# Kernel optimization log

Measured on AMD Instinct MI355X. Metric: run time of the kernel, lower is better.

Reference implementation:

```python
import jax, jax.numpy as jnp
import numpy as np

NHEADS = 16

def setup_inputs() -> dict:
    key = jax.random.key(0)
    ks = jax.random.split(key, 5)
    C = 1024
    d = C // NHEADS
    x  = jax.random.normal(ks[0], (2, 2048, C), dtype=jnp.float32)
    sc = 1.0 / np.sqrt(C)
    wq = jax.random.normal(ks[1], (C, C), dtype=jnp.float32) * sc
    wk = jax.random.normal(ks[2], (C, C), dtype=jnp.float32) * sc
    wv = jax.random.normal(ks[3], (C, C), dtype=jnp.float32) * sc
    wo = jax.random.normal(ks[4], (d, C), dtype=jnp.float32) * (1.0 / np.sqrt(d))
    return {"x": x, "wq": wq, "wk": wk, "wv": wv, "wo": wo}

def reference(x, wq, wk, wv, wo):
    B, T, C = x.shape
    H = NHEADS
    d = C // H

    def split_heads(y):
        return y.reshape(B, T, H, d).transpose(0, 2, 1, 3)  # [B,H,T,d]

    Q = split_heads(x @ wq)
    K = split_heads(x @ wk)
    V = split_heads(x @ wv)

    # scores[b,h,q,k]
    prod = jnp.einsum('bhqd,bhkd->bhqk', Q, K) / np.sqrt(d)

    # ALiBi bias: offset[h, q, k] = (k - q) * 2**(-8*(h+1)/H)
    idx = jnp.arange(T)
    slopes = jnp.exp2(-8.0 * (jnp.arange(H, dtype=jnp.float32) + 1.0) / H)
    bias = (idx[None, :] - idx[:, None]).astype(x.dtype) * slopes[:, None, None]
    prod = prod + bias[None]

    # causal tril mask: keep k <= q
    keep = idx[None, :] <= idx[:, None]  # [T_q, T_k]
    prod = jnp.where(keep[None, None], prod, -jnp.inf)

    # NOTE: original uses F.softmax(prod, 2) -> softmax over the QUERY axis.
    attention_weights = jax.nn.softmax(prod, axis=2)
    attention_output = jnp.einsum('bhqk,bhkd->bhqd', attention_weights, V)

    # per-head wo projection then sum over heads == (sum over heads) @ wo (linear)
    outputs = attention_output.sum(axis=1) @ wo  # [B,T,C]
    return x + outputs
```

## Files before the change

kernel.cpp:

```cpp
#include <hip/hip_runtime.h>
#include <math.h>

#define NB 2
#define NH 16
#define NT 2048
#define ND 64
#define NC 1024
#define L2E 1.44269504f

typedef __attribute__((ext_vector_type(4))) float f32x4;
typedef __attribute__((ext_vector_type(8))) short short8;
typedef __attribute__((ext_vector_type(4))) short short4_t;
typedef __attribute__((ext_vector_type(8))) unsigned short ushort8;
typedef __attribute__((ext_vector_type(4))) unsigned short ushort4_t;

#define GLOAD_LDS(gp, lp)                                                \
    __builtin_amdgcn_global_load_lds(                                    \
        (const __attribute__((address_space(1))) void*)(gp),             \
        (__attribute__((address_space(3))) void*)(lp), 16, 0, 0)

__device__ __forceinline__ int sigma_p(int p) {
    return 4 * ((p >> 3) & 3) + (p & 3) + 16 * ((p >> 2) & 1) + 32 * (p >> 5);
}

__device__ __forceinline__ unsigned short f2bf(float f) {
    unsigned u = __builtin_bit_cast(unsigned, f);
    unsigned r = (u + 0x7FFFu + ((u >> 16) & 1u)) >> 16;
    return (unsigned short)r;
}

__device__ __forceinline__ unsigned cvtpk_bf16(float lo, float hi) {
    unsigned r;
    asm("v_cvt_pk_bf16_f32 %0, %1, %2" : "=v"(r) : "v"(lo), "v"(hi));
    return r;
}

__device__ __forceinline__ f32x4 mfma16(short8 a, short8 b, f32x4 c) {
    return __builtin_amdgcn_mfma_f32_16x16x32_bf16(a, b, c, 0, 0, 0);
}

__device__ __forceinline__ short8 frag_load(const unsigned short* rowp, int g, int half) {
    short8 v;
    short4_t lo = *(const short4_t*)(rowp + 4 * g + 32 * half);
    short4_t hi = *(const short4_t*)(rowp + 4 * g + 16 + 32 * half);
    #pragma unroll
    for (int j = 0; j < 4; ++j) { v[j] = lo[j]; v[4 + j] = hi[j]; }
    return v;
}

__device__ __forceinline__ short8 frag_g(const unsigned short* rowp, int g, int half) {
    return *(const short8*)(rowp + 8 * g + 32 * half);
}

__device__ __forceinline__ short8 frag_swz128(const unsigned short* tile, int row, int g, int half) {
    const char* p = (const char*)tile + row * 128 + (((g + 4 * half) ^ (row & 7)) << 4);
    return *(const short8*)p;
}

__global__ __launch_bounds__(256) void cvt_x(const float* __restrict__ src,
                                             unsigned short* __restrict__ dst, int n4) {
    int i = blockIdx.x * 256 + threadIdx.x;
    if (i >= n4) return;
    const int blk = i >> 4, c4 = i & 15;
    const int gg = (c4 >> 1) & 3, bb = c4 & 1, hh = c4 >> 3;
    f32x4 v = ((const f32x4*)src)[blk * 16 + gg + 4 * bb + 8 * hh];
    ushort4_t o;
    #pragma unroll
    for (int j = 0; j < 4; ++j) o[j] = f2bf(v[j]);
    ((ushort4_t*)dst)[i] = o;
}

__global__ __launch_bounds__(256) void cvtT3(const float* __restrict__ w0,
                                             const float* __restrict__ w1,
                                             const float* __restrict__ w2,
                                             unsigned short* __restrict__ Wt_all) {
    __shared__ __align__(16) float T[64][68];
    const float* W = (blockIdx.z == 0) ? w0 : ((blockIdx.z == 1) ? w1 : w2);
    unsigned short* Wt = Wt_all + (size_t)blockIdx.z * NC * NC;
    const int tid = threadIdx.x;
    const int k0 = blockIdx.x * 64, n0 = blockIdx.y * 64;
    #pragma unroll
    for (int p = 0; p < 4; ++p) {
        int r = 16 * p + (tid >> 4);
        int c = (tid & 15) * 4;
        *(f32x4*)&T[r][c] = *(const f32x4*)&W[(size_t)(k0 + r) * NC + n0 + c];
    }
    __syncthreads();
    const int nr = tid >> 2, kc = (tid & 3) * 16;
    ushort8 o0, o1;
    #pragma unroll
    for (int j = 0; j < 8; ++j) o0[j] = f2bf(T[sigma_p(kc + j)][nr]);
    #pragma unroll
    for (int j = 0; j < 8; ++j) o1[j] = f2bf(T[sigma_p(kc + 8 + j)][nr]);
    unsigned short* q = Wt + (size_t)(n0 + nr) * NC + k0 + kc;
    *(ushort8*)q       = o0;
    *(ushort8*)(q + 8) = o1;
}

__global__ __launch_bounds__(256) void cvtT_wo(const float* __restrict__ W,
                                               unsigned short* __restrict__ Wt) {
    __shared__ __align__(16) float T[64][68];
    const int tid = threadIdx.x;
    const int n0 = blockIdx.y * 64;
    #pragma unroll
    for (int p = 0; p < 4; ++p) {
        int r = 16 * p + (tid >> 4);
        int c = (tid & 15) * 4;
        *(f32x4*)&T[r][c] = *(const f32x4*)&W[(size_t)r * NC + n0 + c];
    }
    __syncthreads();
    const int nr = tid >> 2, kc = (tid & 3) * 16;
    ushort8 o0, o1;
    #pragma unroll
    for (int j = 0; j < 8; ++j) { o0[j] = f2bf(T[kc + j][nr]); o1[j] = f2bf(T[kc + 8 + j][nr]); }
    unsigned short* q = Wt + (size_t)(n0 + nr) * ND + kc;
    *(ushort8*)q       = o0;
    *(ushort8*)(q + 8) = o1;
}

__global__ __launch_bounds__(256) void gemm_qkv(const unsigned short* __restrict__ Xh,
                                                const unsigned short* __restrict__ Wt_all,
                                                unsigned short* __restrict__ dst_all) {
    __shared__ __align__(16) unsigned short Xs[2][8192];
    __shared__ __align__(16) unsigned short Ws[2][8192];
    const int tid = threadIdx.x;
    const int lane = tid & 63, w = tid >> 6;
    const int g = lane >> 4, l15 = lane & 15;
    const int wr = w >> 1, wc = w & 1;
    const int subrow = lane >> 3;
    const int src_off = (((lane & 7) ^ subrow) << 4);
    const int m0 = blockIdx.x * 128;
    const int which = blockIdx.y >> 3;
    const int n0 = (blockIdx.y & 7) * 128;
    const unsigned short* Wt = Wt_all + (size_t)which * NC * NC;
    unsigned short* dst = dst_all + (size_t)which * (NB * NH * NT * ND);

    f32x4 acc[4][4] = {};

    auto stage = [&](int buf, int kk) {
        #pragma unroll
        for (int i = 0; i < 4; ++i) {
            const int r0 = 8 * w + 32 * i;
            const char* xs = (const char*)Xh + (((size_t)(m0 + r0 + subrow) * NC + kk) << 1) + src_off;
            GLOAD_LDS(xs, (char*)&Xs[buf][r0 * 64]);
            const char* ws = (const char*)Wt + (((size_t)(n0 + r0 + subrow) * NC + kk) << 1) + src_off;
            GLOAD_LDS(ws, (char*)&Ws[buf][r0 * 64]);
        }
    };

    stage(0, 0);
    asm volatile("s_waitcnt vmcnt(0)" ::: "memory");
    __builtin_amdgcn_s_barrier();
    int cur = 0;

    for (int kk = 0; kk < NC; kk += 64) {
        if (kk + 64 < NC) stage(cur ^ 1, kk + 64);
        short8 a[4][2], b[4][2];
        #pragma unroll
        for (int mr = 0; mr < 4; ++mr) {
            a[mr][0] = frag_swz128(Xs[cur], 64 * wr + 16 * mr + l15, g, 0);
            a[mr][1] = frag_swz128(Xs[cur], 64 * wr + 16 * mr + l15, g, 1);
        }
        #pragma unroll
        for (int nc = 0; nc < 4; ++nc) {
            b[nc][0] = frag_swz128(Ws[cur], 64 * wc + 16 * nc + l15, g, 0);
            b[nc][1] = frag_swz128(Ws[cur], 64 * wc + 16 * nc + l15, g, 1);
        }
        #pragma unroll
        for (int mr = 0; mr < 4; ++mr)
            #pragma unroll
            for (int nc = 0; nc < 4; ++nc) {
                acc[mr][nc] = mfma16(a[mr][0], b[nc][0], acc[mr][nc]);
                acc[mr][nc] = mfma16(a[mr][1], b[nc][1], acc[mr][nc]);
            }
        asm volatile("s_waitcnt vmcnt(0)" ::: "memory");
        __builtin_amdgcn_s_barrier();
        cur ^= 1;
    }

    #pragma unroll
    for (int mr = 0; mr < 4; ++mr) {
        #pragma unroll
        for (int nc = 0; nc < 4; ++nc) {
            const int n = n0 + 64 * wc + 16 * nc + l15;
            const int hh = n >> 6;
            const int dd = (which < 2)
                ? 32 * (nc >> 1) + 8 * (l15 >> 2) + 4 * (nc & 1) + (l15 & 3)
                : 16 * nc + l15;
            #pragma unroll
            for (int r = 0; r < 4; ++r) {
                const int m = m0 + 64 * wr + 16 * mr + 4 * g + r;
                const int bb = m >> 11, tt = m & (NT - 1);
                dst[(((size_t)bb * NH + hh) * NT + tt) * ND + dd] = f2bf(acc[mr][nc][r]);
            }
        }
    }
}

__global__ __launch_bounds__(256) void transpose_v(const unsigned short* __restrict__ Vh,
                                                   unsigned short* __restrict__ Vt) {
    __shared__ __align__(16) unsigned short T[64][72];
    const int tid = threadIdx.x;
    const int bh = blockIdx.y;
    const int t0 = blockIdx.x * 64;
    const int srow = tid >> 2, scol = (tid & 3) * 16;
    const unsigned short* p = Vh + ((size_t)bh * NT + t0 + srow) * ND + scol;
    *(ushort8*)&T[srow][scol]     = *(const ushort8*)p;
    *(ushort8*)&T[srow][scol + 8] = *(const ushort8*)(p + 8);
    __syncthreads();
    ushort8 o0, o1;
    #pragma unroll
    for (int j = 0; j < 8; ++j) o0[j] = T[sigma_p(scol + j)][srow];
    #pragma unroll
    for (int j = 0; j < 8; ++j) o1[j] = T[sigma_p(scol + 8 + j)][srow];
    unsigned short* q = Vt + ((size_t)bh * ND + srow) * NT + t0 + scol;
    *(ushort8*)q       = o0;
    *(ushort8*)(q + 8) = o1;
}

__global__ __launch_bounds__(256) void colstats(const unsigned short* __restrict__ Qh,
                                                const unsigned short* __restrict__ Kh,
                                                float* __restrict__ Lout) {
    __shared__ __align__(16) unsigned short Qs[3][4096];
    const int tid = threadIdx.x;
    const int lane = tid & 63, w = tid >> 6;
    const int g = lane >> 4, l15 = lane & 15;
    const int subrow = lane >> 3;
    const int src_off = (((lane & 7) ^ subrow) << 4);
    const int lin = blockIdx.x + 16 * blockIdx.y;
    const int xcd = lin & 7, idx = lin >> 3;
    const int bh = xcd * 4 + (idx & 3);
    const int j = idx >> 2;
    const int jA = j, jB = 31 - j;
    const int hh = bh & (NH - 1);
    const float slL2 = exp2f(-0.5f * (float)(hh + 1)) * L2E;
    const float C1 = 0.125f * L2E;
    const float s16 = 16.f * slL2;

    const int K0A = 64 * jA, K0B = 64 * jB;
    const unsigned short* krA = Kh + ((size_t)bh * NT + K0A + 16 * w + l15) * ND;
    const unsigned short* krB = Kh + ((size_t)bh * NT + K0B + 16 * w + l15) * ND;
    const short8 akA0 = frag_g(krA, g, 0), akA1 = frag_g(krA, g, 1);
    const short8 akB0 = frag_g(krB, g, 0), akB1 = frag_g(krB, g, 1);
    const int kA0 = K0A + 16 * w + 4 * g;
    const int kB0 = K0B + 16 * w + 4 * g;

    const char* Qbase = (const char*)(Qh + (size_t)bh * NT * ND);
    auto stage = [&](int buf, int q0) {
        const char* qs = Qbase + (size_t)(q0 + 16 * w + subrow) * 128 + src_off;
        char* qd = (char*)&Qs[buf][16 * w * 64];
        GLOAD_LDS(qs, qd);
        GLOAD_LDS(qs + 1024, qd + 1024);
    };

    f32x4 accA = {}, accB = {};
    float rs[4];
    #pragma unroll
    for (int r = 0; r < 4; ++r) rs[r] = (float)r * slL2;

    stage(0, 64 * jA);
    stage(1, 64 * (jA + 1));
    int cur = 0, nxt = 2;

    auto strip = [&](const short8* qf, const short8& a0, const short8& a1,
                     f32x4& acc, float b0, bool mask) {
        #pragma unroll
        for (int q4 = 0; q4 < 4; ++q4) {
            f32x4 d = {};
            __builtin_amdgcn_s_setprio(1);
            d = mfma16(a0, qf[2 * q4], d);
            d = mfma16(a1, qf[2 * q4 + 1], d);
            __builtin_amdgcn_s_setprio(0);
            #pragma unroll
            for (int r = 0; r < 4; ++r) {
                float e = exp2f(fmaf(d[r], C1, b0 + rs[r]));
                if (mask && (16 * q4 + l15 < 16 * w + 4 * g + r)) e = 0.f;
                acc[r] += e;
            }
            b0 -= s16;
        }
    };

    for (int qt = jA; qt < 32; ++qt) {
        if (qt < 31) asm volatile("s_waitcnt vmcnt(2)" ::: "memory");
        else         asm volatile("s_waitcnt vmcnt(0)" ::: "memory");
        __builtin_amdgcn_s_barrier();
        if (qt + 2 < 32) stage(nxt, 64 * (qt + 2));
        const unsigned short* tile = Qs[cur];
        short8 qf[8];
        #pragma unroll
        for (int q4 = 0; q4 < 4; ++q4) {
            qf[2 * q4]     = frag_swz128(tile, 16 * q4 + l15, g, 0);
            qf[2 * q4 + 1] = frag_swz128(tile, 16 * q4 + l15, g, 1);
        }
        const int q0 = 64 * qt;
        strip(qf, akA0, akA1, accA, (float)(kA0 - q0 - l15) * slL2, qt == jA);
        if (qt >= jB)
            strip(qf, akB0, akB1, accB, (float)(kB0 - q0 - l15) * slL2, qt == jB);
        cur = (cur == 2) ? 0 : cur + 1;
        nxt = (nxt == 2) ? 0 : nxt + 1;
    }
    #pragma unroll
    for (int off = 1; off <= 8; off <<= 1) {
        #pragma unroll
        for (int r = 0; r < 4; ++r) {
            accA[r] += __shfl_xor(accA[r], off);
            accB[r] += __shfl_xor(accB[r], off);
        }
    }
    if (l15 == 0) {
        #pragma unroll
        for (int r = 0; r < 4; ++r) {
            Lout[(size_t)bh * NT + kA0 + r] = log2f(accA[r]);
            Lout[(size_t)bh * NT + kB0 + r] = log2f(accB[r]);
        }
    }
}

__global__ __launch_bounds__(256) void attn_pv(const unsigned short* __restrict__ Qh,
                                               const unsigned short* __restrict__ Kh,
                                               const unsigned short* __restrict__ Vt,
                                               const float* __restrict__ Lc,
                                               float* __restrict__ att) {
    __shared__ __align__(16) unsigned short Ks[3][4096];
    __shared__ __align__(16) unsigned short Vs[3][4096];
    __shared__ __align__(16) float Ls[NT];
    const int tid = threadIdx.x;
    const int lane = tid & 63, w = tid >> 6;
    const int g = lane >> 4, l15 = lane & 15;
    const int subrow = lane >> 3;
    const int src_off = (((lane & 7) ^ subrow) << 4);
    const int lin = blockIdx.x + 16 * blockIdx.y;
    const int xcd = lin & 7, idx = lin >> 3;
    const int bh = xcd * 4 + (idx & 3);
    const int j = idx >> 2;
    const int jA = j, jB = 31 - j;
    const int Q0A = 64 * jA, Q0B = 64 * jB;
    const int qA = Q0A + 16 * w + l15;
    const int qB = Q0B + 16 * w + l15;
    const int hh = bh & (NH - 1);
    const int bb = bh >> 4;
    const float slL2 = exp2f(-0.5f * (float)(hh + 1)) * L2E;
    const float C1 = 0.125f * L2E;

    short8 bqA0, bqA1, bqB0, bqB1;
    {
        const unsigned short* qr = Qh + ((size_t)bh * NT + qA) * ND;
        bqA0 = frag_g(qr, g, 0);
        bqA1 = frag_g(qr, g, 1);
        qr = Qh + ((size_t)bh * NT + qB) * ND;
        bqB0 = frag_g(qr, g, 0);
        bqB1 = frag_g(qr, g, 1);
    }

    auto stageKV = [&](int buf, int K0) {
        const char* ksrc = (const char*)Kh + (size_t)((size_t)bh * NT + K0 + 16 * w + subrow) * 128 + src_off;
        char* kdst = (char*)&Ks[buf][16 * w * 64];
        GLOAD_LDS(ksrc, kdst);
        GLOAD_LDS(ksrc + 1024, kdst + 1024);
        const char* vsrc = (const char*)Vt + ((((size_t)bh * ND + 16 * w + subrow) * NT + K0) << 1) + src_off;
        char* vdst = (char*)&Vs[buf][16 * w * 64];
        GLOAD_LDS(vsrc, vdst);
        GLOAD_LDS(vsrc + 8 * NT * 2, vdst + 1024);
    };

    stageKV(0, 0);
    stageKV(1, 64);
    {
        const f32x4* Lsrc = (const f32x4*)(Lc + (size_t)bh * NT);
        const int nv = (jB + 1) * 16;
        for (int i = tid; i < nv; i += 256) {
            f32x4 v = Lsrc[i];
            float kb = (float)(4 * i);
            #pragma unroll
            for (int c = 0; c < 4; ++c) v[c] -= (kb + (float)c) * slL2;
            ((f32x4*)Ls)[i] = v;
        }
    }
    asm volatile("s_waitcnt lgkmcnt(0)" ::: "memory");
    int cur = 0, nxt = 2;

    f32x4 oA[4] = {}, oB[4] = {};
    const float qsA = (float)qA * slL2;
    const float qsB = (float)qB * slL2;

    auto dostrip = [&](const short8* kf, const short8* vf,
                       const short8& q0f, const short8& q1f, f32x4 (&o)[4],
                       float qsc, int q, int K0, bool mask) {
        f32x4 pacc[4];
        __builtin_amdgcn_s_setprio(1);
        #pragma unroll
        for (int s4 = 0; s4 < 4; ++s4) {
            f32x4 d = {};
            d = mfma16(kf[2 * s4], q0f, d);
            d = mfma16(kf[2 * s4 + 1], q1f, d);
            pacc[s4] = d;
        }
        __builtin_amdgcn_s_setprio(0);
        union { unsigned u[4]; short8 s; } pa[2];
        #pragma unroll
        for (int s4 = 0; s4 < 4; ++s4) {
            f32x4 Lf = *(const f32x4*)&Ls[K0 + 16 * s4 + 4 * g];
            float p[4];
            #pragma unroll
            for (int r = 0; r < 4; ++r)
                p[r] = exp2f(fmaf(pacc[s4][r], C1, -(Lf[r] + qsc)));
            if (mask) {
                #pragma unroll
                for (int r = 0; r < 4; ++r)
                    if (K0 + 16 * s4 + 4 * g + r > q) p[r] = 0.f;
            }
            pa[s4 >> 1].u[2 * (s4 & 1)]     = cvtpk_bf16(p[0], p[1]);
            pa[s4 >> 1].u[2 * (s4 & 1) + 1] = cvtpk_bf16(p[2], p[3]);
        }
        __builtin_amdgcn_s_setprio(1);
        #pragma unroll
        for (int n = 0; n < 4; ++n) {
            o[n] = mfma16(pa[0].s, vf[2 * n], o[n]);
            o[n] = mfma16(pa[1].s, vf[2 * n + 1], o[n]);
        }
        __builtin_amdgcn_s_setprio(0);
    };

    for (int kt = 0; kt <= jB; ++kt) {
        if (kt < jB) asm volatile("s_waitcnt vmcnt(4)" ::: "memory");
        else         asm volatile("s_waitcnt vmcnt(0)" ::: "memory");
        __builtin_amdgcn_s_barrier();
        if (kt + 2 <= jB) stageKV(nxt, 64 * (kt + 2));
        const int K0 = 64 * kt;
        short8 kf[8], vf[8];
        #pragma unroll
        for (int s4 = 0; s4 < 4; ++s4) {
            kf[2 * s4]     = frag_swz128(Ks[cur], 16 * s4 + l15, g, 0);
            kf[2 * s4 + 1] = frag_swz128(Ks[cur], 16 * s4 + l15, g, 1);
            vf[2 * s4]     = frag_swz128(Vs[cur], 16 * s4 + l15, g, 0);
            vf[2 * s4 + 1] = frag_swz128(Vs[cur], 16 * s4 + l15, g, 1);
        }
        dostrip(kf, vf, bqB0, bqB1, oB, qsB, qB, K0, kt == jB);
        if (kt <= jA)
            dostrip(kf, vf, bqA0, bqA1, oA, qsA, qA, K0, kt == jA);
        cur = (cur == 2) ? 0 : cur + 1;
        nxt = (nxt == 2) ? 0 : nxt + 1;
    }
    #pragma unroll
    for (int n = 0; n < 4; ++n) {
        #pragma unroll
        for (int r = 0; r < 4; ++r) {
            att[(((size_t)bb * NT + Q0A + 16 * w + 4 * g + r) * NH + hh) * ND + 16 * n + l15] = oA[n][r];
            att[(((size_t)bb * NT + Q0B + 16 * w + 4 * g + r) * NH + hh) * ND + 16 * n + l15] = oB[n][r];
        }
    }
}

__global__ __launch_bounds__(256) void headsum(const float* __restrict__ att,
                                               unsigned short* __restrict__ A) {
    const int row = blockIdx.x * 16 + (threadIdx.x >> 4);
    const int d0 = (threadIdx.x & 15) * 4;
    const float* p = att + (size_t)row * (NH * ND) + d0;
    f32x4 s = {};
    #pragma unroll
    for (int h = 0; h < NH; ++h) {
        f32x4 v = *(const f32x4*)(p + h * ND);
        s += v;
    }
    ushort4_t o;
    #pragma unroll
    for (int j = 0; j < 4; ++j) o[j] = f2bf(s[j]);
    *(ushort4_t*)&A[(size_t)row * ND + d0] = o;
}

__global__ __launch_bounds__(256) void out_proj(const float* __restrict__ x,
                                                const unsigned short* __restrict__ A,
                                                const unsigned short* __restrict__ Wot,
                                                float* __restrict__ out) {
    const int tid = threadIdx.x;
    const int lane = tid & 63, w = tid >> 6;
    const int g = lane >> 4, l15 = lane & 15;
    const int m0 = blockIdx.x * 64, n0 = blockIdx.y * 64;

    const unsigned short* ar = A + (size_t)(m0 + 16 * w + l15) * ND;
    short8 a0 = frag_load(ar, g, 0);
    short8 a1 = frag_load(ar, g, 1);

    f32x4 acc[4] = {};
    #pragma unroll
    for (int ns = 0; ns < 4; ++ns) {
        const unsigned short* br = Wot + (size_t)(n0 + 16 * ns + l15) * ND;
        acc[ns] = mfma16(a0, frag_load(br, g, 0), acc[ns]);
        acc[ns] = mfma16(a1, frag_load(br, g, 1), acc[ns]);
    }
    #pragma unroll
    for (int ns = 0; ns < 4; ++ns) {
        #pragma unroll
        for (int r = 0; r < 4; ++r) {
            int m = m0 + 16 * w + 4 * g + r;
            int n = n0 + 16 * ns + l15;
            out[(size_t)m * NC + n] = x[(size_t)m * NC + n] + acc[ns][r];
        }
    }
}

extern "C" void kernel_launch(void* const* d_in, const int* in_sizes, int n_in,
                              void* d_out, int out_size, void* d_ws, size_t ws_size,
                              hipStream_t stream) {
    const float* x  = (const float*)d_in[0];
    const float* wq = (const float*)d_in[1];
    const float* wk = (const float*)d_in[2];
    const float* wv = (const float*)d_in[3];
    const float* wo = (const float*)d_in[4];
    float* out = (float*)d_out;

    const size_t MB = 1u << 20;
    const size_t KB = 1u << 10;
    unsigned char* w8 = (unsigned char*)d_ws;
    unsigned short* Xh  = (unsigned short*)(w8);
    unsigned short* Wta = (unsigned short*)(w8 + 8 * MB);
    unsigned short* Qh  = (unsigned short*)(w8 + 14 * MB);
    unsigned short* Kh  = (unsigned short*)(w8 + 22 * MB);
    unsigned short* Vh  = (unsigned short*)(w8 + 30 * MB);
    unsigned short* Vt  = (unsigned short*)(w8 + 38 * MB);
    float*          att = (float*)(w8 + 46 * MB);
    float*          Lc  = (float*)(w8 + 62 * MB);
    unsigned short* A   = (unsigned short*)(w8 + 62 * MB + 256 * KB);
    unsigned short* Wot = (unsigned short*)(w8 + 62 * MB + 768 * KB);

    cvt_x<<<(NB * NT * NC) / 1024, 256, 0, stream>>>(x, Xh, (NB * NT * NC) / 4);
    cvtT3<<<dim3(16, 16, 3), 256, 0, stream>>>(wq, wk, wv, Wta);
    cvtT_wo<<<dim3(1, 16), 256, 0, stream>>>(wo, Wot);

    gemm_qkv<<<dim3(32, 24), 256, 0, stream>>>(Xh, Wta, Qh);

    transpose_v<<<dim3(32, 32), 256, 0, stream>>>(Vh, Vt);

    colstats<<<dim3(16, 32), 256, 0, stream>>>(Qh, Kh, Lc);
    attn_pv<<<dim3(16, 32), 256, 0, stream>>>(Qh, Kh, Vt, Lc, att);

    headsum<<<(NB * NT) / 16, 256, 0, stream>>>(att, A);
    out_proj<<<dim3(64, 16), 256, 0, stream>>>(x, A, Wot, out);
}
```

Before: 151.3 us.

## Fuse V transpose into QKV GEMM epilogue and split attention loops by parity

The QKV GEMM now writes V straight into the transposed, permuted layout that attention expects, which removes the separate transpose_v kernel and its extra round trip through memory. Both colstats and attn_pv double their grids and split the reduction loop into even and odd tiles. Partial column sums are combined with log2 inside attn_pv, and the two partial attention outputs are added in headsum. attn_pv drops to double buffering with a full barrier each iteration and requests occupancy 4, trading deeper prefetch for more parallel blocks and extra partial-output traffic.

```diff
diff --git a/kernel.cpp b/kernel.cpp
--- a/kernel.cpp
+++ b/kernel.cpp
@@ -120,7 +120,8 @@
 
 __global__ __launch_bounds__(256) void gemm_qkv(const unsigned short* __restrict__ Xh,
                                                 const unsigned short* __restrict__ Wt_all,
-                                                unsigned short* __restrict__ dst_all) {
+                                                unsigned short* __restrict__ qk_dst,
+                                                unsigned short* __restrict__ Vt) {
     __shared__ __align__(16) unsigned short Xs[2][8192];
     __shared__ __align__(16) unsigned short Ws[2][8192];
     const int tid = threadIdx.x;
@@ -133,7 +134,6 @@
     const int which = blockIdx.y >> 3;
     const int n0 = (blockIdx.y & 7) * 128;
     const unsigned short* Wt = Wt_all + (size_t)which * NC * NC;
-    unsigned short* dst = dst_all + (size_t)which * (NB * NH * NT * ND);
 
     f32x4 acc[4][4] = {};
 
@@ -178,59 +178,56 @@
         cur ^= 1;
     }
 
-    #pragma unroll
-    for (int mr = 0; mr < 4; ++mr) {
-        #pragma unroll
-        for (int nc = 0; nc < 4; ++nc) {
-            const int n = n0 + 64 * wc + 16 * nc + l15;
-            const int hh = n >> 6;
-            const int dd = (which < 2)
-                ? 32 * (nc >> 1) + 8 * (l15 >> 2) + 4 * (nc & 1) + (l15 & 3)
-                : 16 * nc + l15;
+    if (which < 2) {
+        unsigned short* dst = qk_dst + (size_t)which * (NB * NH * NT * ND);
+        #pragma unroll
+        for (int mr = 0; mr < 4; ++mr) {
             #pragma unroll
-            for (int r = 0; r < 4; ++r) {
-                const int m = m0 + 64 * wr + 16 * mr + 4 * g + r;
-                const int bb = m >> 11, tt = m & (NT - 1);
-                dst[(((size_t)bb * NH + hh) * NT + tt) * ND + dd] = f2bf(acc[mr][nc][r]);
+            for (int nc = 0; nc < 4; ++nc) {
+                const int n = n0 + 64 * wc + 16 * nc + l15;
+                const int hh = n >> 6;
+                const int dd = 32 * (nc >> 1) + 8 * (l15 >> 2) + 4 * (nc & 1) + (l15 & 3);
+                #pragma unroll
+                for (int r = 0; r < 4; ++r) {
+                    const int m = m0 + 64 * wr + 16 * mr + 4 * g + r;
+                    const int bb = m >> 11, tt = m & (NT - 1);
+                    dst[(((size_t)bb * NH + hh) * NT + tt) * ND + dd] = f2bf(acc[mr][nc][r]);
+                }
             }
         }
-    }
-}
-
-__global__ __launch_bounds__(256) void transpose_v(const unsigned short* __restrict__ Vh,
-                                                   unsigned short* __restrict__ Vt) {
-    __shared__ __align__(16) unsigned short T[64][72];
-    const int tid = threadIdx.x;
-    const int bh = blockIdx.y;
-    const int t0 = blockIdx.x * 64;
-    const int srow = tid >> 2, scol = (tid & 3) * 16;
-    const unsigned short* p = Vh + ((size_t)bh * NT + t0 + srow) * ND + scol;
-    *(ushort8*)&T[srow][scol]     = *(const ushort8*)p;
-    *(ushort8*)&T[srow][scol + 8] = *(const ushort8*)(p + 8);
-    __syncthreads();
-    ushort8 o0, o1;
-    #pragma unroll
-    for (int j = 0; j < 8; ++j) o0[j] = T[sigma_p(scol + j)][srow];
-    #pragma unroll
-    for (int j = 0; j < 8; ++j) o1[j] = T[sigma_p(scol + 8 + j)][srow];
-    unsigned short* q = Vt + ((size_t)bh * ND + srow) * NT + t0 + scol;
-    *(ushort8*)q       = o0;
-    *(ushort8*)(q + 8) = o1;
-}
-
-__global__ __launch_bounds__(256) void colstats(const unsigned short* __restrict__ Qh,
-                                                const unsigned short* __restrict__ Kh,
-                                                float* __restrict__ Lout) {
+    } else {
+        #pragma unroll
+        for (int mr = 0; mr < 4; ++mr) {
+            const int m = m0 + 64 * wr + 16 * mr + 4 * g;
+            const int bb = m >> 11, tt = m & (NT - 1);
+            const int tbase = (tt & ~63) + 32 * (mr >> 1) + 8 * g + 4 * (mr & 1);
+            #pragma unroll
+            for (int nc = 0; nc < 4; ++nc) {
+                const int n = n0 + 64 * wc + 16 * nc + l15;
+                const int hh = n >> 6, dd = n & 63;
+                ushort4_t o;
+                #pragma unroll
+                for (int r = 0; r < 4; ++r) o[r] = f2bf(acc[mr][nc][r]);
+                *(ushort4_t*)&Vt[(((size_t)bb * NH + hh) * ND + dd) * NT + tbase] = o;
+            }
+        }
+    }
+}
+
+__global__ __launch_bounds__(256, 4) void colstats(const unsigned short* __restrict__ Qh,
+                                                   const unsigned short* __restrict__ Kh,
+                                                   float* __restrict__ Lc2) {
     __shared__ __align__(16) unsigned short Qs[3][4096];
     const int tid = threadIdx.x;
     const int lane = tid & 63, w = tid >> 6;
     const int g = lane >> 4, l15 = lane & 15;
     const int subrow = lane >> 3;
     const int src_off = (((lane & 7) ^ subrow) << 4);
-    const int lin = blockIdx.x + 16 * blockIdx.y;
+    const int lin = blockIdx.x + 32 * blockIdx.y;
     const int xcd = lin & 7, idx = lin >> 3;
     const int bh = xcd * 4 + (idx & 3);
-    const int j = idx >> 2;
+    const int rest = idx >> 2;
+    const int j = rest >> 1, par = rest & 1;
     const int jA = j, jB = 31 - j;
     const int hh = bh & (NH - 1);
     const float slL2 = exp2f(-0.5f * (float)(hh + 1)) * L2E;
@@ -258,8 +255,9 @@
     #pragma unroll
     for (int r = 0; r < 4; ++r) rs[r] = (float)r * slL2;
 
-    stage(0, 64 * jA);
-    stage(1, 64 * (jA + 1));
+    const int qt0 = jA + ((par ^ jA) & 1);
+    stage(0, 64 * qt0);
+    stage(1, 64 * (qt0 + 2));
     int cur = 0, nxt = 2;
 
     auto strip = [&](const short8* qf, const short8& a0, const short8& a1,
@@ -281,11 +279,11 @@
         }
     };
 
-    for (int qt = jA; qt < 32; ++qt) {
-        if (qt < 31) asm volatile("s_waitcnt vmcnt(2)" ::: "memory");
-        else         asm volatile("s_waitcnt vmcnt(0)" ::: "memory");
+    for (int qt = qt0; qt < 32; qt += 2) {
+        if (qt + 2 < 32) asm volatile("s_waitcnt vmcnt(2)" ::: "memory");
+        else             asm volatile("s_waitcnt vmcnt(0)" ::: "memory");
         __builtin_amdgcn_s_barrier();
-        if (qt + 2 < 32) stage(nxt, 64 * (qt + 2));
+        if (qt + 4 < 32) stage(nxt, 64 * (qt + 4));
         const unsigned short* tile = Qs[cur];
         short8 qf[8];
         #pragma unroll
@@ -309,31 +307,34 @@
         }
     }
     if (l15 == 0) {
+        float* Lp = Lc2 + (size_t)(par * 32 + bh) * NT;
         #pragma unroll
         for (int r = 0; r < 4; ++r) {
-            Lout[(size_t)bh * NT + kA0 + r] = log2f(accA[r]);
-            Lout[(size_t)bh * NT + kB0 + r] = log2f(accB[r]);
-        }
-    }
-}
-
-__global__ __launch_bounds__(256) void attn_pv(const unsigned short* __restrict__ Qh,
-                                               const unsigned short* __restrict__ Kh,
-                                               const unsigned short* __restrict__ Vt,
-                                               const float* __restrict__ Lc,
-                                               float* __restrict__ att) {
-    __shared__ __align__(16) unsigned short Ks[3][4096];
-    __shared__ __align__(16) unsigned short Vs[3][4096];
+            Lp[kA0 + r] = accA[r];
+            Lp[kB0 + r] = accB[r];
+        }
+    }
+}
+
+__global__ __launch_bounds__(256, 4) void attn_pv(const unsigned short* __restrict__ Qh,
+                                                  const unsigned short* __restrict__ Kh,
+                                                  const unsigned short* __restrict__ Vt,
+                                                  const float* __restrict__ Lc2,
+                                                  float* __restrict__ att_a,
+                                                  float* __restrict__ att_b) {
+    __shared__ __align__(16) unsigned short Ks[2][4096];
+    __shared__ __align__(16) unsigned short Vs[2][4096];
     __shared__ __align__(16) float Ls[NT];
     const int tid = threadIdx.x;
     const int lane = tid & 63, w = tid >> 6;
     const int g = lane >> 4, l15 = lane & 15;
     const int subrow = lane >> 3;
     const int src_off = (((lane & 7) ^ subrow) << 4);
-    const int lin = blockIdx.x + 16 * blockIdx.y;
+    const int lin = blockIdx.x + 32 * blockIdx.y;
     const int xcd = lin & 7, idx = lin >> 3;
     const int bh = xcd * 4 + (idx & 3);
-    const int j = idx >> 2;
+    const int rest = idx >> 2;
+    const int j = rest >> 1, par = rest & 1;
     const int jA = j, jB = 31 - j;
     const int Q0A = 64 * jA, Q0B = 64 * jB;
     const int qA = Q0A + 16 * w + l15;
@@ -364,21 +365,25 @@
         GLOAD_LDS(vsrc + 8 * NT * 2, vdst + 1024);
     };
 
-    stageKV(0, 0);
-    stageKV(1, 64);
+    const int kt0 = par;
+    stageKV(0, 64 * kt0);
     {
-        const f32x4* Lsrc = (const f32x4*)(Lc + (size_t)bh * NT);
+        const f32x4* La = (const f32x4*)(Lc2 + (size_t)bh * NT);
+        const f32x4* Lb = (const f32x4*)(Lc2 + (size_t)(32 + bh) * NT);
         const int nv = (jB + 1) * 16;
         for (int i = tid; i < nv; i += 256) {
-            f32x4 v = Lsrc[i];
+            f32x4 a = La[i], b = Lb[i];
             float kb = (float)(4 * i);
+            f32x4 v;
             #pragma unroll
-            for (int c = 0; c < 4; ++c) v[c] -= (kb + (float)c) * slL2;
+            for (int c = 0; c < 4; ++c)
+                v[c] = log2f(a[c] + b[c]) - (kb + (float)c) * slL2;
             ((f32x4*)Ls)[i] = v;
         }
     }
-    asm volatile("s_waitcnt lgkmcnt(0)" ::: "memory");
-    int cur = 0, nxt = 2;
+    asm volatile("s_waitcnt vmcnt(0) lgkmcnt(0)" ::: "memory");
+    __builtin_amdgcn_s_barrier();
+    int cur = 0;
 
     f32x4 oA[4] = {}, oB[4] = {};
     const float qsA = (float)qA * slL2;
@@ -422,11 +427,8 @@
         __builtin_amdgcn_s_setprio(0);
     };
 
-    for (int kt = 0; kt <= jB; ++kt) {
-        if (kt < jB) asm volatile("s_waitcnt vmcnt(4)" ::: "memory");
-        else         asm volatile("s_waitcnt vmcnt(0)" ::: "memory");
-        __builtin_amdgcn_s_barrier();
-        if (kt + 2 <= jB) stageKV(nxt, 64 * (kt + 2));
+    for (int kt = kt0; kt <= jB; kt += 2) {
+        if (kt + 2 <= jB) stageKV(cur ^ 1, 64 * (kt + 2));
         const int K0 = 64 * kt;
         short8 kf[8], vf[8];
         #pragma unroll
@@ -439,9 +441,11 @@
         dostrip(kf, vf, bqB0, bqB1, oB, qsB, qB, K0, kt == jB);
         if (kt <= jA)
             dostrip(kf, vf, bqA0, bqA1, oA, qsA, qA, K0, kt == jA);
-        cur = (cur == 2) ? 0 : cur + 1;
-        nxt = (nxt == 2) ? 0 : nxt + 1;
-    }
+        asm volatile("s_waitcnt vmcnt(0)" ::: "memory");
+        __builtin_amdgcn_s_barrier();
+        cur ^= 1;
+    }
+    float* att = (par == 0) ? att_a : att_b;
     #pragma unroll
     for (int n = 0; n < 4; ++n) {
         #pragma unroll
@@ -452,16 +456,18 @@
     }
 }
 
-__global__ __launch_bounds__(256) void headsum(const float* __restrict__ att,
+__global__ __launch_bounds__(256) void headsum(const float* __restrict__ att_a,
+                                               const float* __restrict__ att_b,
                                                unsigned short* __restrict__ A) {
     const int row = blockIdx.x * 16 + (threadIdx.x >> 4);
     const int d0 = (threadIdx.x & 15) * 4;
-    const float* p = att + (size_t)row * (NH * ND) + d0;
+    const float* pa = att_a + (size_t)row * (NH * ND) + d0;
+    const float* pb = att_b + (size_t)row * (NH * ND) + d0;
     f32x4 s = {};
     #pragma unroll
     for (int h = 0; h < NH; ++h) {
-        f32x4 v = *(const f32x4*)(p + h * ND);
-        s += v;
+        s += *(const f32x4*)(pa + h * ND);
+        s += *(const f32x4*)(pb + h * ND);
     }
     ushort4_t o;
     #pragma unroll
@@ -513,28 +519,26 @@
     const size_t MB = 1u << 20;
     const size_t KB = 1u << 10;
     unsigned char* w8 = (unsigned char*)d_ws;
-    unsigned short* Xh  = (unsigned short*)(w8);
-    unsigned short* Wta = (unsigned short*)(w8 + 8 * MB);
-    unsigned short* Qh  = (unsigned short*)(w8 + 14 * MB);
-    unsigned short* Kh  = (unsigned short*)(w8 + 22 * MB);
-    unsigned short* Vh  = (unsigned short*)(w8 + 30 * MB);
-    unsigned short* Vt  = (unsigned short*)(w8 + 38 * MB);
-    float*          att = (float*)(w8 + 46 * MB);
-    float*          Lc  = (float*)(w8 + 62 * MB);
-    unsigned short* A   = (unsigned short*)(w8 + 62 * MB + 256 * KB);
-    unsigned short* Wot = (unsigned short*)(w8 + 62 * MB + 768 * KB);
+    unsigned short* Xh    = (unsigned short*)(w8);
+    unsigned short* Wta   = (unsigned short*)(w8 + 8 * MB);
+    unsigned short* Qh    = (unsigned short*)(w8 + 16 * MB);
+    unsigned short* Kh    = (unsigned short*)(w8 + 24 * MB);
+    unsigned short* Vt    = (unsigned short*)(w8 + 32 * MB);
+    float*          att_a = (float*)(w8 + 40 * MB);
+    float*          att_b = (float*)(w8);
+    float*          Lc2   = (float*)(w8 + 56 * MB);
+    unsigned short* A     = (unsigned short*)(w8 + 56 * MB + 512 * KB);
+    unsigned short* Wot   = (unsigned short*)(w8 + 57 * MB);
 
     cvt_x<<<(NB * NT * NC) / 1024, 256, 0, stream>>>(x, Xh, (NB * NT * NC) / 4);
     cvtT3<<<dim3(16, 16, 3), 256, 0, stream>>>(wq, wk, wv, Wta);
     cvtT_wo<<<dim3(1, 16), 256, 0, stream>>>(wo, Wot);
 
-    gemm_qkv<<<dim3(32, 24), 256, 0, stream>>>(Xh, Wta, Qh);
-
-    transpose_v<<<dim3(32, 32), 256, 0, stream>>>(Vh, Vt);
-
-    colstats<<<dim3(16, 32), 256, 0, stream>>>(Qh, Kh, Lc);
-    attn_pv<<<dim3(16, 32), 256, 0, stream>>>(Qh, Kh, Vt, Lc, att);
-
-    headsum<<<(NB * NT) / 16, 256, 0, stream>>>(att, A);
+    gemm_qkv<<<dim3(32, 24), 256, 0, stream>>>(Xh, Wta, Qh, Vt);
+
+    colstats<<<dim3(32, 32), 256, 0, stream>>>(Qh, Kh, Lc2);
+    attn_pv<<<dim3(32, 32), 256, 0, stream>>>(Qh, Kh, Vt, Lc2, att_a, att_b);
+
+    headsum<<<(NB * NT) / 16, 256, 0, stream>>>(att_a, att_b, A);
     out_proj<<<dim3(64, 16), 256, 0, stream>>>(x, A, Wot, out);
 }
```

New measurement: 179.9 us, median of 2. +18.9%, slower.
